# Kernel tuning notes

Hardware: AMD Instinct MI355X
Metric: run time of the kernel (lower is better)

## Reference

```python
import jax, jax.numpy as jnp
import numpy as np

S, B, W, H = 97, 256, 1024, 16
HD = W // H


def setup_inputs() -> dict:
    key = jax.random.key(0)
    ks = jax.random.split(key, 16)
    def p(k, shape):
        return jax.random.normal(k, shape, jnp.float32) * 0.02
    return {
        "tensor": jax.random.normal(ks[0], (S, B, W), jnp.float32),
        "mask": jnp.zeros((S, S), jnp.float32),
        "q_w": p(ks[1], (W, W)), "q_b": p(ks[2], (W,)),
        "k_w": p(ks[3], (W, W)), "k_b": p(ks[4], (W,)),
        "v_w": p(ks[5], (W, W)), "v_b": p(ks[6], (W,)),
        "in_proj_w": p(ks[7], (3 * W, W)), "in_proj_b": p(ks[8], (3 * W,)),
        "mha_out_w": p(ks[9], (W, W)), "mha_out_b": p(ks[10], (W,)),
        "out_w": p(ks[11], (W, W)), "out_b": p(ks[12], (W,)),
    }


def _freqs_cos_sin(dim, seqlen, theta=10000.0):
    # matches precompute_freqs_cis: angle[t, j] = t / theta**(2j/dim)
    inv = 1.0 / (theta ** (jnp.arange(0, dim, 2, dtype=jnp.float32) / dim))  # (dim/2,)
    ang = jnp.arange(seqlen, dtype=jnp.float32)[:, None] * inv[None, :]      # (S, dim/2)
    return jnp.cos(ang)[:, None, :], jnp.sin(ang)[:, None, :]                # (S, 1, dim/2)


def _rotary(x, cos, sin):
    # x: (S, B, D); pairs (even, odd) along last dim form complex numbers
    s, b, d = x.shape
    xr = x.reshape(s, b, d // 2, 2)
    xe, xo = xr[..., 0], xr[..., 1]
    oe = xe * cos - xo * sin
    oo = xe * sin + xo * cos
    return jnp.stack([oe, oo], axis=-1).reshape(s, b, d)


def reference(tensor, mask, q_w, q_b, k_w, k_b, v_w, v_b,
              in_proj_w, in_proj_b, mha_out_w, mha_out_b, out_w, out_b):
    # tensor: (S, B, W) -- torch MHA default batch_first=False layout
    q = tensor @ q_w.T + q_b
    k = tensor @ k_w.T + k_b
    v = tensor @ v_w.T + v_b

    cos, sin = _freqs_cos_sin(W, S)
    q = _rotary(q, cos, sin)
    k = _rotary(k, cos, sin)

    # nn.MultiheadAttention internal in_proj (applied on top of q/k/v linears)
    Wq, Wk, Wv = in_proj_w[:W], in_proj_w[W:2 * W], in_proj_w[2 * W:]
    bq, bk, bv = in_proj_b[:W], in_proj_b[W:2 * W], in_proj_b[2 * W:]
    q = q @ Wq.T + bq
    k = k @ Wk.T + bk
    v = v @ Wv.T + bv

    def split_heads(x):  # (S,B,W) -> (B,H,S,HD)
        return x.reshape(S, B, H, HD).transpose(1, 2, 0, 3)

    qh, kh, vh = split_heads(q), split_heads(k), split_heads(v)
    scale = 1.0 / jnp.sqrt(jnp.float32(HD))
    scores = jnp.einsum('bhqd,bhkd->bhqk', qh, kh) * scale + mask  # additive float mask
    attn = jax.nn.softmax(scores, axis=-1)
    o = jnp.einsum('bhqk,bhkd->bhqd', attn, vh)      # (B,H,S,HD)
    o = o.transpose(2, 0, 1, 3).reshape(S, B, W)     # (S,B,W)
    o = o @ mha_out_w.T + mha_out_b                  # MHA out_proj
    return o @ out_w.T + out_b                       # module's final self.out
```

## Files before the change

kernel.cpp:

```cpp
#include <hip/hip_runtime.h>
#include <cstdint>
#include <cstddef>

#define S_LEN 97
#define B_DIM 256
#define W_DIM 1024
#define NH    16
#define HDIM  64
#define MROWS (S_LEN * B_DIM)

typedef unsigned short u16;
typedef __bf16 bf16x8 __attribute__((ext_vector_type(8)));
typedef float  f32x4  __attribute__((ext_vector_type(4)));

__device__ __forceinline__ u16 f2bf(float f) {
  union { float f; uint32_t u; } v; v.f = f;
  uint32_t u = v.u;
  return (u16)((u + 0x7FFFu + ((u >> 16) & 1u)) >> 16);
}
__device__ __forceinline__ float bf2f(u16 h) {
  union { uint32_t u; float f; } v; v.u = ((uint32_t)h) << 16;
  return v.f;
}

__device__ __forceinline__ void gload16(const void* g, void* lds) {
  __builtin_amdgcn_global_load_lds(
      (const __attribute__((address_space(1))) void*)(uintptr_t)g,
      (__attribute__((address_space(3))) void*)(uint32_t)(uintptr_t)lds,
      16, 0, 0);
}

__global__ void k_cvt(const float* __restrict__ s, u16* __restrict__ d, int n4) {
  int i = blockIdx.x * blockDim.x + threadIdx.x;
  if (i >= n4) return;
  float4 v = ((const float4*)s)[i];
  uint2 pk;
  pk.x = (uint32_t)f2bf(v.x) | ((uint32_t)f2bf(v.y) << 16);
  pk.y = (uint32_t)f2bf(v.z) | ((uint32_t)f2bf(v.w) << 16);
  ((uint2*)d)[i] = pk;
}

__global__ void k_cvt_t(const float* __restrict__ src, u16* __restrict__ dst) {
  __shared__ float t[32][33];
  const int bx = blockIdx.x * 32, by = blockIdx.y * 32;
  const int tx = threadIdx.x, ty = threadIdx.y;
  for (int yy = ty; yy < 32; yy += 8)
    t[yy][tx] = src[(size_t)(by + yy) * 1024 + bx + tx];
  __syncthreads();
  for (int yy = ty; yy < 32; yy += 8)
    dst[(size_t)(bx + yy) * 1024 + by + tx] = f2bf(t[tx][yy]);
}

__global__ void k_bias2(const float* a, const float* b, float* dst) {
  int i = blockIdx.x * blockDim.x + threadIdx.x;
  if (i >= 2 * W_DIM) return;
  dst[i] = (i < W_DIM) ? a[i] : b[i - W_DIM];
}

__global__ void k_zero(float* dst, int n) {
  int i = blockIdx.x * blockDim.x + threadIdx.x;
  if (i < n) dst[i] = 0.f;
}

__global__ void k_maskpad(const float* __restrict__ mask, float* __restrict__ mp) {
  int i = blockIdx.x * blockDim.x + threadIdx.x;
  int r = i >> 7, c = i & 127;
  float v;
  if (c >= S_LEN) v = -1e30f;
  else if (r < S_LEN) v = mask[r * S_LEN + c];
  else v = 0.f;
  mp[i] = v;
}

__global__ void k_biasfold(const float* __restrict__ M, const float* __restrict__ v,
                           const float* __restrict__ b2, float* __restrict__ out) {
  const int lane = threadIdx.x & 63, wave = threadIdx.x >> 6;
  const int row = blockIdx.x * 4 + wave;
  float s = 0.f;
  for (int k = lane; k < 1024; k += 64) s += M[(size_t)row * 1024 + k] * v[k];
#pragma unroll
  for (int d = 32; d; d >>= 1) s += __shfl_xor(s, d);
  if (lane == 0) out[row] = s + b2[row];
}

__global__ void k_rope_tab(float* __restrict__ tab) {
  int idx = blockIdx.x * blockDim.x + threadIdx.x;
  if (idx >= S_LEN * 512) return;
  int s = idx / 512, i = idx % 512;
  float freq = expf(-(float)i * (9.210340371976184f / 512.0f));
  float ang = (float)s * freq;
  float sv, cv;
  sincosf(ang, &sv, &cv);
  tab[idx * 2 + 0] = cv;
  tab[idx * 2 + 1] = sv;
}

template <int OUT_MODE>
__global__ __launch_bounds__(256) void k_gemm(
    const u16* __restrict__ A, int lda, const u16* __restrict__ Bw,
    const float* __restrict__ bias, void* __restrict__ Cp, int ldc, int K) {
  __shared__ u16 As[128 * 64];
  __shared__ u16 Bs[128 * 64];

  const int tid = threadIdx.x, lane = tid & 63, wave = tid >> 6;
  const int wm = wave >> 1, wn = wave & 1;
  const int m0 = blockIdx.y * 128;
  const int n0 = blockIdx.x * 128;

  f32x4 acc[4][4] = {};

  const int lrow = lane >> 3;
  const int lcol = (lane & 7) * 8;
  const u16* Ag = A + (size_t)(m0 + wave * 8 + lrow) * lda + lcol;
  const u16* Bg = Bw + (size_t)(n0 + wave * 8 + lrow) * K + lcol;
  u16* Asl = As + wave * 8 * 64;
  u16* Bsl = Bs + wave * 8 * 64;

  for (int kt = 0; kt < K; kt += 64) {
#pragma unroll
    for (int i = 0; i < 4; ++i) {
      gload16(Ag + (size_t)(i * 32) * lda + kt, Asl + i * 2048);
      gload16(Bg + (size_t)(i * 32) * K + kt, Bsl + i * 2048);
    }
    __syncthreads();
#pragma unroll
    for (int kk = 0; kk < 2; ++kk) {
      bf16x8 af[4], bfr[4];
#pragma unroll
      for (int m = 0; m < 4; ++m)
        af[m] = *(const bf16x8*)(As + (wm * 64 + m * 16 + (lane & 15)) * 64 + kk * 32 + (lane >> 4) * 8);
#pragma unroll
      for (int n = 0; n < 4; ++n)
        bfr[n] = *(const bf16x8*)(Bs + (wn * 64 + n * 16 + (lane & 15)) * 64 + kk * 32 + (lane >> 4) * 8);
#pragma unroll
      for (int m = 0; m < 4; ++m)
#pragma unroll
        for (int n = 0; n < 4; ++n)
          acc[m][n] = __builtin_amdgcn_mfma_f32_16x16x32_bf16(af[m], bfr[n], acc[m][n], 0, 0, 0);
    }
    __syncthreads();
  }

  const int r0 = (lane >> 4) * 4;
  const int c0 = lane & 15;
#pragma unroll
  for (int m = 0; m < 4; ++m) {
#pragma unroll
    for (int n = 0; n < 4; ++n) {
      const int col = n0 + wn * 64 + n * 16 + c0;
      const float bv = bias[col];
#pragma unroll
      for (int r = 0; r < 4; ++r) {
        const int row = m0 + wm * 64 + m * 16 + r0 + r;
        const float v = acc[m][n][r] + bv;
        if (OUT_MODE == 0) {
          ((u16*)Cp)[(size_t)row * ldc + col] = f2bf(v);
        } else if (OUT_MODE == 2) {
          ((float*)Cp)[(size_t)row * ldc + col] = v;
        }
      }
    }
  }
}

template <int OUT_MODE, int ACOLB, int SCALEQ = 0>
__global__ __launch_bounds__(512, 2) void k_gemm256(
    const u16* __restrict__ A, int lda, const u16* __restrict__ Bw,
    const float* __restrict__ bias, void* __restrict__ Cp, int ldc,
    size_t thirdStride, const float* __restrict__ tab, int Nt) {
  __shared__ u16 lds[2 * 32768];

  const int tid = threadIdx.x, lane = tid & 63, wave = tid >> 6;
  const int wm = wave >> 2, wn = wave & 3;
  const int c0 = lane & 15, hi = lane >> 4;

  const int nwg = gridDim.x;
  const int qq = nwg >> 3, rr_ = nwg & 7;
  const int xcd = blockIdx.x & 7, sub = blockIdx.x >> 3;
  const int seq = (xcd < rr_ ? xcd * (qq + 1) : rr_ * (qq + 1) + (xcd - rr_) * qq) + sub;
  const int mt = seq / Nt, nt = seq - mt * Nt;
  const int m0 = mt * 256, n0 = nt * 256;
  const int aoff = ACOLB ? (n0 & ~1023) : 0;

  const int rl = tid >> 3, pc = tid & 7;
  const int gc = pc ^ (rl & 7);
  const u16* aS = A + (size_t)(m0 + rl) * lda + aoff + gc * 8;
  const u16* bS = Bw + (size_t)(n0 + rl) * 1024 + gc * 8;
  const uint32_t ldsW = wave * 512;

  auto stageR = [&](int tt, int L) {
    const int bb = (tt & 1) * 32768;
    const u16* src = (L < 4) ? (aS + (size_t)(L * 64) * lda + tt * 64)
                             : (bS + (size_t)((L - 4) * 64) * 1024 + tt * 64);
    gload16(src, (u16*)lds + bb + L * 4096 + ldsW);
  };

  int aofr[2][8], bofr[2][4];
#pragma unroll
  for (int kk = 0; kk < 2; ++kk) {
#pragma unroll
    for (int m = 0; m < 8; ++m)
      aofr[kk][m] = (wm * 128 + m * 16 + c0) * 64 + (((kk * 4 + hi) ^ (c0 & 7)) * 8);
#pragma unroll
    for (int n = 0; n < 4; ++n)
      bofr[kk][n] = 16384 + (wn * 64 + n * 16 + c0) * 64 + (((kk * 4 + hi) ^ (c0 & 7)) * 8);
  }

  stageR(0, 0); stageR(0, 2); stageR(0, 4); stageR(0, 5);
  stageR(0, 6); stageR(0, 7); stageR(0, 1); stageR(0, 3);
  asm volatile("s_waitcnt vmcnt(2)" ::: "memory");
  __builtin_amdgcn_s_barrier();

  f32x4 acc[8][4] = {};
  bf16x8 bfr[4], af[4];

#define MFMA16(MB)                                                              \
  _Pragma("unroll") for (int m = 0; m < 4; ++m)                                 \
  _Pragma("unroll") for (int n = 0; n < 4; ++n)                                 \
      acc[(MB) + m][n] =                                                        \
          __builtin_amdgcn_mfma_f32_16x16x32_bf16(af[m], bfr[n], acc[(MB) + m][n], 0, 0, 0);

#define PH_MID()                                                 \
  __builtin_amdgcn_s_barrier();                                  \
  asm volatile("s_waitcnt lgkmcnt(0)" ::: "memory");             \
  __builtin_amdgcn_sched_barrier(0);                             \
  __builtin_amdgcn_s_setprio(1);

#define PH_END()                                                 \
  __builtin_amdgcn_s_setprio(0);                                 \
  __builtin_amdgcn_sched_barrier(0);

  for (int t = 0; t < 16; ++t) {
    const u16* buf = lds + (t & 1) * 32768;
    const bool pf = (t < 15);

#pragma unroll
    for (int n = 0; n < 4; ++n) bfr[n] = *(const bf16x8*)(buf + bofr[0][n]);
#pragma unroll
    for (int m = 0; m < 4; ++m) af[m] = *(const bf16x8*)(buf + aofr[0][m]);
    if (pf) { stageR(t + 1, 0); stageR(t + 1, 2); }
    PH_MID();
    MFMA16(0);
    PH_END();
    if (pf) asm volatile("s_waitcnt vmcnt(2)" ::: "memory");
    else    asm volatile("s_waitcnt vmcnt(0)" ::: "memory");
    __builtin_amdgcn_s_barrier();

#pragma unroll
    for (int m = 0; m < 4; ++m) af[m] = *(const bf16x8*)(buf + aofr[0][4 + m]);
    if (pf) { stageR(t + 1, 4); stageR(t + 1, 5); }
    PH_MID();
    MFMA16(4);
    PH_END();
    __builtin_amdgcn_s_barrier();

#pragma unroll
    for (int n = 0; n < 4; ++n) bfr[n] = *(const bf16x8*)(buf + bofr[1][n]);
#pragma unroll
    for (int m = 0; m < 4; ++m) af[m] = *(const bf16x8*)(buf + aofr[1][m]);
    if (pf) { stageR(t + 1, 6); stageR(t + 1, 7); }
    PH_MID();
    MFMA16(0);
    PH_END();
    __builtin_amdgcn_s_barrier();

#pragma unroll
    for (int m = 0; m < 4; ++m) af[m] = *(const bf16x8*)(buf + aofr[1][4 + m]);
    if (pf) { stageR(t + 1, 1); stageR(t + 1, 3); }
    PH_MID();
    MFMA16(4);
    PH_END();
    if (pf) asm volatile("s_waitcnt vmcnt(2)" ::: "memory");
    __builtin_amdgcn_s_barrier();
  }
#undef MFMA16
#undef PH_MID
#undef PH_END

  const int r0 = (lane >> 4) * 4;
#pragma unroll
  for (int m = 0; m < 8; ++m) {
#pragma unroll
    for (int n = 0; n < 4; ++n) {
      const int col = n0 + wn * 64 + n * 16 + c0;
      const float bv = bias[col];
      if (OUT_MODE == 3) {
        const int pairI = (col & 1023) >> 1;
        const float sgn = (col & 1) ? 1.f : -1.f;
#pragma unroll
        for (int r = 0; r < 4; ++r) {
          const int row = m0 + wm * 128 + m * 16 + r0 + r;
          const float v = acc[m][n][r] + bv;
          const float p = __shfl_xor(v, 1);
          const float2 cs = ((const float2*)tab)[(row >> 8) * 512 + pairI];
          ((u16*)Cp)[(size_t)row * ldc + col] = f2bf(v * cs.x + sgn * p * cs.y);
        }
      } else {
#pragma unroll
        for (int r = 0; r < 4; ++r) {
          const int row = m0 + wm * 128 + m * 16 + r0 + r;
          const float v = acc[m][n][r] + bv;
          if (OUT_MODE == 0) {
            ((u16*)Cp)[(size_t)row * ldc + col] = f2bf(v);
          } else if (OUT_MODE == 2) {
            ((float*)Cp)[(size_t)row * ldc + col] = v;
          } else {
            const int which = col >> 10, c = col & 1023;
            const int h = c >> 6, d = c & 63;
            const int s = row >> 8, b = row & 255;
            const float sc = (SCALEQ && which == 0) ? 0.125f : 1.0f;
            ((u16*)Cp)[(size_t)which * thirdStride +
                       (((size_t)(b * NH + h) * S_LEN + s) * HDIM + d)] = f2bf(v * sc);
          }
        }
      }
    }
  }
}

__global__ __launch_bounds__(512, 6) void k_attn(const u16* __restrict__ qkv2,
                                                 const float* __restrict__ maskP,
                                                 u16* __restrict__ O1) {
  __shared__ u16 Vt[64 * 128];
  __shared__ u16 Pb[128 * 128];
  __shared__ float redM[4][128];
  __shared__ float redS[4][128];

  const size_t TS = (size_t)MROWS * W_DIM;
  const int bh = blockIdx.x, b = bh >> 4, h = bh & 15;
  const int tid = threadIdx.x, lane = tid & 63, wave = tid >> 6;
  const int wm = wave >> 2;
  const int wn = wave & 3;
  const int c0 = lane & 15, hi = lane >> 4;

  const u16* Qg = qkv2 + (size_t)bh * (S_LEN * HDIM);
  const u16* Kg = Qg + TS;
  const u16* Vg = Qg + 2 * TS;

  for (int idx = tid; idx < 1024; idx += 512) {
    const int s = idx >> 3, c = (idx & 7) * 8;
    uint4 vv = make_uint4(0, 0, 0, 0);
    if (s < S_LEN) vv = *(const uint4*)(Vg + (size_t)s * HDIM + c);
    u16 tmp[8];
    *(uint4*)tmp = vv;
#pragma unroll
    for (int j = 0; j < 8; ++j)
      Vt[(c + j) * 128 + (s ^ (j << 3))] = tmp[j];
  }

  f32x4 acc[4][2] = {};
#pragma unroll
  for (int kk = 0; kk < 2; ++kk) {
    bf16x8 af[4], bfr[2];
#pragma unroll
    for (int m = 0; m < 4; ++m)
      af[m] = *(const bf16x8*)(Qg + (size_t)(wm * 64 + m * 16 + c0) * HDIM + kk * 32 + hi * 8);
#pragma unroll
    for (int n = 0; n < 2; ++n)
      bfr[n] = *(const bf16x8*)(Kg + (size_t)(wn * 32 + n * 16 + c0) * HDIM + kk * 32 + hi * 8);
#pragma unroll
    for (int m = 0; m < 4; ++m)
#pragma unroll
      for (int n = 0; n < 2; ++n)
        acc[m][n] = __builtin_amdgcn_mfma_f32_16x16x32_bf16(af[m], bfr[n], acc[m][n], 0, 0, 0);
  }

#pragma unroll
  for (int m = 0; m < 4; ++m) {
    float mxm[4];
#pragma unroll
    for (int r = 0; r < 4; ++r) {
      const int row = wm * 64 + m * 16 + hi * 4 + r;
#pragma unroll
      for (int n = 0; n < 2; ++n)
        acc[m][n][r] += maskP[row * 128 + wn * 32 + n * 16 + c0];
      mxm[r] = fmaxf(acc[m][0][r], acc[m][1][r]);
    }
#pragma unroll
    for (int d = 1; d < 16; d <<= 1)
#pragma unroll
      for (int r = 0; r < 4; ++r)
        mxm[r] = fmaxf(mxm[r], __shfl_xor(mxm[r], d));
    if (c0 == 0) {
#pragma unroll
      for (int r = 0; r < 4; ++r)
        redM[wn][wm * 64 + m * 16 + hi * 4 + r] = mxm[r];
    }
  }
  __syncthreads();

#pragma unroll
  for (int m = 0; m < 4; ++m) {
    float psm[4];
#pragma unroll
    for (int r = 0; r < 4; ++r) {
      const int row = wm * 64 + m * 16 + hi * 4 + r;
      const float rm = fmaxf(fmaxf(redM[0][row], redM[1][row]),
                             fmaxf(redM[2][row], redM[3][row]));
      float p = 0.f;
#pragma unroll
      for (int n = 0; n < 2; ++n) {
        const float e = __expf(acc[m][n][r] - rm);
        p += e;
        const int col = wn * 32 + n * 16 + c0;
        Pb[row * 128 + (col ^ ((row & 7) << 3))] = f2bf(e);
      }
      psm[r] = p;
    }
#pragma unroll
    for (int d = 1; d < 16; d <<= 1)
#pragma unroll
      for (int r = 0; r < 4; ++r)
        psm[r] += __shfl_xor(psm[r], d);
    if (c0 == 0) {
#pragma unroll
      for (int r = 0; r < 4; ++r)
        redS[wn][wm * 64 + m * 16 + hi * 4 + r] = psm[r];
    }
  }
  __syncthreads();

  f32x4 o[4] = {};
#pragma unroll
  for (int kk = 0; kk < 4; ++kk) {
    bf16x8 pa[4], vb;
#pragma unroll
    for (int m = 0; m < 4; ++m) {
      const int row = wm * 64 + m * 16 + c0;
      pa[m] = *(const bf16x8*)(Pb + row * 128 + ((kk * 32 + hi * 8) ^ ((row & 7) << 3)));
    }
    {
      const int d = wn * 16 + c0;
      vb = *(const bf16x8*)(Vt + d * 128 + ((kk * 32 + hi * 8) ^ ((d & 7) << 3)));
    }
#pragma unroll
    for (int m = 0; m < 4; ++m)
      o[m] = __builtin_amdgcn_mfma_f32_16x16x32_bf16(pa[m], vb, o[m], 0, 0, 0);
  }

#pragma unroll
  for (int m = 0; m < 4; ++m)
#pragma unroll
    for (int r = 0; r < 4; ++r) {
      const int row = wm * 64 + m * 16 + hi * 4 + r;
      if (row < S_LEN) {
        const float iv = 1.0f / (redS[0][row] + redS[1][row] + redS[2][row] + redS[3][row]);
        const int d = wn * 16 + c0;
        O1[((size_t)row * B_DIM + b) * W_DIM + h * HDIM + d] = f2bf(o[m][r] * iv);
      }
    }
}

extern "C" void kernel_launch(void* const* d_in, const int* in_sizes, int n_in,
                              void* d_out, int out_size, void* d_ws, size_t ws_size,
                              hipStream_t stream) {
  (void)in_sizes; (void)n_in; (void)out_size; (void)ws_size;
  const float* tensor    = (const float*)d_in[0];
  const float* mask      = (const float*)d_in[1];
  const float* q_w       = (const float*)d_in[2];
  const float* q_b       = (const float*)d_in[3];
  const float* k_w       = (const float*)d_in[4];
  const float* k_b       = (const float*)d_in[5];
  const float* v_w       = (const float*)d_in[6];
  const float* v_b       = (const float*)d_in[7];
  const float* in_proj_w = (const float*)d_in[8];
  const float* in_proj_b = (const float*)d_in[9];
  const float* mha_w     = (const float*)d_in[10];
  const float* mha_b     = (const float*)d_in[11];
  const float* out_w     = (const float*)d_in[12];
  const float* out_b     = (const float*)d_in[13];

  char* ws = (char*)d_ws;
  size_t off = 0;
  auto alloc = [&](size_t bytes) {
    char* p = ws + off;
    off += (bytes + 255) & ~(size_t)255;
    return p;
  };

  const size_t TS = (size_t)MROWS * W_DIM;

  float* tab = (float*)alloc((size_t)S_LEN * 512 * 2 * sizeof(float));
  float* maskP = (float*)alloc((size_t)128 * 128 * sizeof(float));
  u16* Xbf   = (u16*)alloc(TS * 2);
  u16* qkv1  = (u16*)alloc((size_t)MROWS * 2048 * 2);
  u16* qkv2  = (u16*)alloc(TS * 3 * 2);
  u16* WC1   = (u16*)alloc((size_t)2048 * 1024 * 2);
  u16* W2    = (u16*)alloc((size_t)3072 * 1024 * 2);
  u16* WvT   = (u16*)alloc((size_t)1024 * 1024 * 2);
  u16* WmT   = (u16*)alloc((size_t)1024 * 1024 * 2);
  u16* WO    = (u16*)alloc((size_t)1024 * 1024 * 2);
  u16* WVf   = (u16*)alloc((size_t)1024 * 1024 * 2);
  u16* WFf   = (u16*)alloc((size_t)1024 * 1024 * 2);
  float* bc1 = (float*)alloc(2048 * sizeof(float));
  float* bvf = (float*)alloc(1024 * sizeof(float));
  float* bff = (float*)alloc(1024 * sizeof(float));
  float* zb  = (float*)alloc(1024 * sizeof(float));
  u16* O1 = Xbf;

  k_rope_tab<<<dim3((S_LEN * 512 + 255) / 256), 256, 0, stream>>>(tab);
  k_maskpad<<<dim3(64), 256, 0, stream>>>(mask, maskP);
  k_cvt<<<dim3(MROWS * W_DIM / 4 / 256), 256, 0, stream>>>(tensor, Xbf, MROWS * W_DIM / 4);
  k_cvt<<<dim3(1024), 256, 0, stream>>>(q_w, WC1, 262144);
  k_cvt<<<dim3(1024), 256, 0, stream>>>(k_w, WC1 + 1048576, 262144);
  k_cvt<<<dim3(3072), 256, 0, stream>>>(in_proj_w, W2, 786432);
  k_cvt<<<dim3(1024), 256, 0, stream>>>(out_w, WO, 262144);
  k_cvt_t<<<dim3(32, 32), dim3(32, 8), 0, stream>>>(v_w, WvT);
  k_cvt_t<<<dim3(32, 32), dim3(32, 8), 0, stream>>>(mha_w, WmT);
  k_bias2<<<dim3(8), 256, 0, stream>>>(q_b, k_b, bc1);
  k_zero<<<dim3(4), 256, 0, stream>>>(zb, 1024);
  k_biasfold<<<dim3(256), 256, 0, stream>>>(in_proj_w + (size_t)2048 * 1024, v_b,
                                            in_proj_b + 2048, bvf);
  k_biasfold<<<dim3(256), 256, 0, stream>>>(out_w, mha_b, out_b, bff);

  k_gemm<0><<<dim3(8, 8), 256, 0, stream>>>(
      W2 + (size_t)2048 * 1024, 1024, WvT, zb, WVf, 1024, 1024);
  k_gemm<0><<<dim3(8, 8), 256, 0, stream>>>(
      WO, 1024, WmT, zb, WFf, 1024, 1024);

  k_gemm256<3, 0><<<dim3(97 * 8), 512, 0, stream>>>(
      Xbf, W_DIM, WC1, bc1, qkv1, 2048, 0, tab, 8);

  k_gemm256<1, 0><<<dim3(97 * 4), 512, 0, stream>>>(
      Xbf, W_DIM, WVf, bvf, qkv2 + 2 * TS, 0, TS, nullptr, 4);

  k_gemm256<1, 1, 1><<<dim3(97 * 8), 512, 0, stream>>>(
      qkv1, 2048, W2, in_proj_b, qkv2, 0, TS, nullptr, 8);

  k_attn<<<dim3(B_DIM * NH), 512, 0, stream>>>(qkv2, maskP, O1);

  k_gemm256<2, 0><<<dim3(97 * 4), 512, 0, stream>>>(
      O1, W_DIM, WFf, bff, d_out, W_DIM, 0, nullptr, 4);
}
```

Baseline: 614.7 us.

## Double-buffer GEMM fragments in registers and use one barrier per K-step

```diff
diff --git a/kernel.cpp b/kernel.cpp
--- a/kernel.cpp
+++ b/kernel.cpp
@@ -206,76 +206,70 @@
       bofr[kk][n] = 16384 + (wn * 64 + n * 16 + c0) * 64 + (((kk * 4 + hi) ^ (c0 & 7)) * 8);
   }
 
-  stageR(0, 0); stageR(0, 2); stageR(0, 4); stageR(0, 5);
-  stageR(0, 6); stageR(0, 7); stageR(0, 1); stageR(0, 3);
-  asm volatile("s_waitcnt vmcnt(2)" ::: "memory");
+  stageR(0, 0); stageR(0, 1); stageR(0, 2); stageR(0, 3);
+  stageR(0, 4); stageR(0, 5); stageR(0, 6); stageR(0, 7);
+  asm volatile("s_waitcnt vmcnt(0)" ::: "memory");
   __builtin_amdgcn_s_barrier();
 
   f32x4 acc[8][4] = {};
-  bf16x8 bfr[4], af[4];
-
-#define MFMA16(MB)                                                              \
+  bf16x8 afP[4], afN[4], bfrC[4], bfrN[4];
+
+  {
+    const u16* buf = lds;
+#pragma unroll
+    for (int n = 0; n < 4; ++n) bfrC[n] = *(const bf16x8*)(buf + bofr[0][n]);
+#pragma unroll
+    for (int m = 0; m < 4; ++m) afP[m] = *(const bf16x8*)(buf + aofr[0][m]);
+  }
+
+#define MFMA16(MB, AF, BF)                                                      \
   _Pragma("unroll") for (int m = 0; m < 4; ++m)                                 \
   _Pragma("unroll") for (int n = 0; n < 4; ++n)                                 \
       acc[(MB) + m][n] =                                                        \
-          __builtin_amdgcn_mfma_f32_16x16x32_bf16(af[m], bfr[n], acc[(MB) + m][n], 0, 0, 0);
-
-#define PH_MID()                                                 \
-  __builtin_amdgcn_s_barrier();                                  \
-  asm volatile("s_waitcnt lgkmcnt(0)" ::: "memory");             \
-  __builtin_amdgcn_sched_barrier(0);                             \
-  __builtin_amdgcn_s_setprio(1);
-
-#define PH_END()                                                 \
-  __builtin_amdgcn_s_setprio(0);                                 \
-  __builtin_amdgcn_sched_barrier(0);
+          __builtin_amdgcn_mfma_f32_16x16x32_bf16(AF[m], BF[n], acc[(MB) + m][n], 0, 0, 0);
 
   for (int t = 0; t < 16; ++t) {
     const u16* buf = lds + (t & 1) * 32768;
+    const u16* nbuf = lds + ((t + 1) & 1) * 32768;
     const bool pf = (t < 15);
 
 #pragma unroll
-    for (int n = 0; n < 4; ++n) bfr[n] = *(const bf16x8*)(buf + bofr[0][n]);
-#pragma unroll
-    for (int m = 0; m < 4; ++m) af[m] = *(const bf16x8*)(buf + aofr[0][m]);
-    if (pf) { stageR(t + 1, 0); stageR(t + 1, 2); }
-    PH_MID();
-    MFMA16(0);
-    PH_END();
-    if (pf) asm volatile("s_waitcnt vmcnt(2)" ::: "memory");
-    else    asm volatile("s_waitcnt vmcnt(0)" ::: "memory");
-    __builtin_amdgcn_s_barrier();
-
-#pragma unroll
-    for (int m = 0; m < 4; ++m) af[m] = *(const bf16x8*)(buf + aofr[0][4 + m]);
-    if (pf) { stageR(t + 1, 4); stageR(t + 1, 5); }
-    PH_MID();
-    MFMA16(4);
-    PH_END();
-    __builtin_amdgcn_s_barrier();
-
-#pragma unroll
-    for (int n = 0; n < 4; ++n) bfr[n] = *(const bf16x8*)(buf + bofr[1][n]);
-#pragma unroll
-    for (int m = 0; m < 4; ++m) af[m] = *(const bf16x8*)(buf + aofr[1][m]);
-    if (pf) { stageR(t + 1, 6); stageR(t + 1, 7); }
-    PH_MID();
-    MFMA16(0);
-    PH_END();
-    __builtin_amdgcn_s_barrier();
-
-#pragma unroll
-    for (int m = 0; m < 4; ++m) af[m] = *(const bf16x8*)(buf + aofr[1][4 + m]);
+    for (int m = 0; m < 4; ++m) afN[m] = *(const bf16x8*)(buf + aofr[0][4 + m]);
+    if (pf) { stageR(t + 1, 0); stageR(t + 1, 2); stageR(t + 1, 4); }
+    __builtin_amdgcn_s_setprio(1);
+    MFMA16(0, afP, bfrC);
+    __builtin_amdgcn_s_setprio(0);
+
+#pragma unroll
+    for (int n = 0; n < 4; ++n) bfrN[n] = *(const bf16x8*)(buf + bofr[1][n]);
+#pragma unroll
+    for (int m = 0; m < 4; ++m) afP[m] = *(const bf16x8*)(buf + aofr[1][m]);
+    if (pf) { stageR(t + 1, 5); stageR(t + 1, 6); stageR(t + 1, 7); }
+    __builtin_amdgcn_s_setprio(1);
+    MFMA16(4, afN, bfrC);
+    __builtin_amdgcn_s_setprio(0);
+
+#pragma unroll
+    for (int m = 0; m < 4; ++m) afN[m] = *(const bf16x8*)(buf + aofr[1][4 + m]);
     if (pf) { stageR(t + 1, 1); stageR(t + 1, 3); }
-    PH_MID();
-    MFMA16(4);
-    PH_END();
-    if (pf) asm volatile("s_waitcnt vmcnt(2)" ::: "memory");
-    __builtin_amdgcn_s_barrier();
+    __builtin_amdgcn_s_setprio(1);
+    MFMA16(0, afP, bfrN);
+    __builtin_amdgcn_s_setprio(0);
+
+    __builtin_amdgcn_s_setprio(1);
+    MFMA16(4, afN, bfrN);
+    __builtin_amdgcn_s_setprio(0);
+
+    if (pf) {
+      asm volatile("s_waitcnt vmcnt(0)" ::: "memory");
+      __builtin_amdgcn_s_barrier();
+#pragma unroll
+      for (int n = 0; n < 4; ++n) bfrC[n] = *(const bf16x8*)(nbuf + bofr[0][n]);
+#pragma unroll
+      for (int m = 0; m < 4; ++m) afP[m] = *(const bf16x8*)(nbuf + aofr[0][m]);
+    }
   }
 #undef MFMA16
-#undef PH_MID
-#undef PH_END
 
   const int r0 = (lane >> 4) * 4;
 #pragma unroll
```

Result: no change. 608.2 us (-1.1%).
